# Optimization experiments

Measured on AMD Instinct MI355X. Metric: run time of the kernel, lower is better.

## Reference

```python
import jax, jax.numpy as jnp
import numpy as np

DIM = 3072
NUM_HEADS = 24
HEAD_DIM = DIM // NUM_HEADS        # 128
B = 1
F, H, W = 4, 24, 24
S = F * H * W                      # 2304
EPS = 1e-6
MAX_POS = 1024
C2 = HEAD_DIM // 2                 # 64 rotary channel-pairs per head
CF = C2 - 2 * (C2 // 3)            # 22 pairs for frame axis
CH = C2 // 3                       # 21 pairs each for H and W axes


def rmsnorm(x, g, eps=EPS):
    # fp32 RMSNorm over last dim with affine weight g [DIM]
    xf = x.astype(jnp.float32)
    ms = jnp.mean(xf * xf, axis=-1, keepdims=True)
    return (xf * jax.lax.rsqrt(ms + eps) * g).astype(x.dtype)


def apply_default_rope(x, grid_sizes, freqs):
    # x: [B, S, N, D]; freqs: [1024, C2] angle table; grid_sizes: [B,3] (F,H,W)
    b, s, n, d = x.shape
    gh = grid_sizes[0, 1]
    gw = grid_sizes[0, 2]
    pos = jnp.arange(s)
    fi = pos // (gh * gw)
    hi = (pos % (gh * gw)) // gw
    wi = pos % gw
    # per-position angles, split across (F, H, W) channel groups -> [S, C2]
    theta = jnp.concatenate([
        freqs[fi, :CF],
        freqs[hi, CF:CF + CH],
        freqs[wi, CF + CH:],
    ], axis=-1)
    cos = jnp.cos(theta)[None, :, None, :]
    sin = jnp.sin(theta)[None, :, None, :]
    xp = x.astype(jnp.float32).reshape(b, s, n, d // 2, 2)
    xr, xi = xp[..., 0], xp[..., 1]
    out = jnp.stack([xr * cos - xi * sin, xr * sin + xi * cos], axis=-1)
    return out.reshape(b, s, n, d).astype(x.dtype)


def setup_inputs() -> dict:
    key = jax.random.key(0)
    ks = jax.random.split(key, 10)
    def w(k):
        return jax.random.normal(k, (DIM, DIM), dtype=jnp.float32) * 0.02
    inv = 10000.0 ** (-jnp.arange(C2, dtype=jnp.float32) / C2)
    freqs = jnp.arange(MAX_POS, dtype=jnp.float32)[:, None] * inv[None, :]
    return {
        "x": jax.random.normal(ks[0], (B, S, DIM), dtype=jnp.float32),
        "seq_lens": jnp.full((B,), S, dtype=jnp.int32),
        "grid_sizes": jnp.tile(jnp.array([[F, H, W]], dtype=jnp.int32), (B, 1)),
        "freqs": freqs,
        "wq": w(ks[1]), "bq": jnp.zeros((DIM,), jnp.float32),
        "wk": w(ks[2]), "bk": jnp.zeros((DIM,), jnp.float32),
        "wv": w(ks[3]), "bv": jnp.zeros((DIM,), jnp.float32),
        "wo": w(ks[4]), "bo": jnp.zeros((DIM,), jnp.float32),
        "gq": jnp.ones((DIM,), jnp.float32),
        "gk": jnp.ones((DIM,), jnp.float32),
    }


def reference(x, seq_lens, grid_sizes, freqs, wq, bq, wk, bk, wv, bv, wo, bo, gq, gk):
    b, s = x.shape[:2]
    n, d = NUM_HEADS, HEAD_DIM
    # QKV projections (torch Linear: x @ W.T + b) + fp32 RMSNorm on q, k
    q = rmsnorm(x @ wq.T + bq, gq).reshape(b, s, n, d)
    k = rmsnorm(x @ wk.T + bk, gk).reshape(b, s, n, d)
    v = (x @ wv.T + bv).reshape(b, s, n, d)
    # 3-axis (F,H,W) RoPE on q, k
    q = apply_default_rope(q, grid_sizes, freqs)
    k = apply_default_rope(k, grid_sizes, freqs)
    # non-causal attention with k_lens masking
    scores = jnp.einsum('bqnd,bknd->bnqk', q, k) * (d ** -0.5)
    kmask = jnp.arange(s)[None, :] < seq_lens[:, None]          # [B, S]
    scores = jnp.where(kmask[:, None, None, :], scores, -1e9)
    probs = jax.nn.softmax(scores, axis=-1)
    out = jnp.einsum('bnqk,bknd->bqnd', probs, v).reshape(b, s, n * d)
    return out @ wo.T + bo
```

## Files before the change

### kernel.cpp

```cpp
#include <hip/hip_runtime.h>
#include <hip/hip_bf16.h>
#include <cstdint>

#define S_LEN 2304
#define NDIM  3072
#define NH    24
#define HD    128

typedef unsigned short u16;
typedef __bf16  bf16x8  __attribute__((ext_vector_type(8)));
typedef float   floatx4 __attribute__((ext_vector_type(4)));

__device__ __forceinline__ u16 f2bf(float x) {
  union { float f; unsigned int u; } a; a.f = x;
  unsigned int r = (a.u + 0x7FFFu + ((a.u >> 16) & 1u)) >> 16;
  return (u16)r;
}

__device__ __forceinline__ void async_load16(const void* g, void* l) {
  auto gp = (const __attribute__((address_space(1))) unsigned int*)(unsigned long long)(g);
  auto lp = (__attribute__((address_space(3))) unsigned int*)(unsigned int)(unsigned long long)(l);
  __builtin_amdgcn_global_load_lds(gp, lp, 16, 0, 0);
}

__global__ __launch_bounds__(256) void cvt_all(const float* __restrict__ x,
                                               const float* __restrict__ w0,
                                               const float* __restrict__ w1,
                                               const float* __restrict__ w2,
                                               const float* __restrict__ w3,
                                               u16* __restrict__ xo,
                                               u16* __restrict__ o0,
                                               u16* __restrict__ o1,
                                               u16* __restrict__ o2,
                                               u16* __restrict__ o3) {
  long b = blockIdx.x;
  const float* in; u16* out;
  if (b < 3456) { in = x; out = xo; }
  else {
    long wi = (b - 3456) / 4608;
    b = (b - 3456) % 4608;
    in  = (wi == 0) ? w0 : (wi == 1) ? w1 : (wi == 2) ? w2 : w3;
    out = (wi == 0) ? o0 : (wi == 1) ? o1 : (wi == 2) ? o2 : o3;
  }
  long i = (b * 256 + threadIdx.x) * 8;
  float4 a = *(const float4*)(in + i);
  float4 c = *(const float4*)(in + i + 4);
  union { u16 h[8]; uint4 u; } r;
  r.h[0] = f2bf(a.x); r.h[1] = f2bf(a.y); r.h[2] = f2bf(a.z); r.h[3] = f2bf(a.w);
  r.h[4] = f2bf(c.x); r.h[5] = f2bf(c.y); r.h[6] = f2bf(c.z); r.h[7] = f2bf(c.w);
  *(uint4*)(out + i) = r.u;
}

__device__ __forceinline__ void gemm_tile(const u16* __restrict__ A,
                                          const u16* __restrict__ B,
                                          const float* __restrict__ bias,
                                          float* __restrict__ C,
                                          int bm, int bn,
                                          u16* As, u16* Bs) {
  constexpr int N = NDIM, K = NDIM;
  const int t = threadIdx.x;
  const int l = t & 63, w = t >> 6;
  const int l15 = l & 15, quad = l >> 4;
  const int wm = (w >> 1) * 64, wn = (w & 1) * 64;

  floatx4 acc[4][4];
#pragma unroll
  for (int i = 0; i < 4; ++i)
#pragma unroll
    for (int j = 0; j < 4; ++j) acc[i][j] = {0.f, 0.f, 0.f, 0.f};

  for (int kt = 0; kt < K / 64; ++kt) {
    const int k0 = kt * 64;
#pragma unroll
    for (int i = 0; i < 4; ++i) {
      int p = i * 256 + t;
      int r = p >> 3;
      int c = (p & 7) ^ (r & 7);
      async_load16(A + (long)(bm + r) * K + k0 + c * 8, As + p * 8);
      async_load16(B + (long)(bn + r) * K + k0 + c * 8, Bs + p * 8);
    }
    __syncthreads();
#pragma unroll
    for (int kk = 0; kk < 2; ++kk) {
      bf16x8 af[4], bfr[4];
#pragma unroll
      for (int i = 0; i < 4; ++i) {
        int row = wm + i * 16 + l15;
        int cc = kk * 4 + quad;
        af[i] = *(const bf16x8*)(As + (row * 8 + (cc ^ (row & 7))) * 8);
      }
#pragma unroll
      for (int j = 0; j < 4; ++j) {
        int row = wn + j * 16 + l15;
        int cc = kk * 4 + quad;
        bfr[j] = *(const bf16x8*)(Bs + (row * 8 + (cc ^ (row & 7))) * 8);
      }
#pragma unroll
      for (int i = 0; i < 4; ++i)
#pragma unroll
        for (int j = 0; j < 4; ++j)
          acc[i][j] = __builtin_amdgcn_mfma_f32_16x16x32_bf16(af[i], bfr[j], acc[i][j], 0, 0, 0);
    }
    __syncthreads();
  }
#pragma unroll
  for (int i = 0; i < 4; ++i)
#pragma unroll
    for (int j = 0; j < 4; ++j) {
      int gm = bm + wm + i * 16 + quad * 4;
      int gn = bn + wn + j * 16 + l15;
      float bv = bias[gn];
#pragma unroll
      for (int r = 0; r < 4; ++r)
        C[(long)(gm + r) * N + gn] = acc[i][j][r] + bv;
    }
}

__global__ __launch_bounds__(256, 2) void gemm_qkv(const u16* __restrict__ A,
                                                   const u16* __restrict__ wq,
                                                   const u16* __restrict__ wk,
                                                   const u16* __restrict__ wv,
                                                   const float* __restrict__ bq,
                                                   const float* __restrict__ bk,
                                                   const float* __restrict__ bv,
                                                   float* __restrict__ qf,
                                                   float* __restrict__ kf,
                                                   float* __restrict__ vf) {
  __shared__ u16 As[128 * 64];
  __shared__ u16 Bs[128 * 64];
  const int sel = blockIdx.x / 24;
  const int bn = (blockIdx.x % 24) * 128;
  const int bm = blockIdx.y * 128;
  const u16*   B    = (sel == 0) ? wq : (sel == 1) ? wk : wv;
  const float* bias = (sel == 0) ? bq : (sel == 1) ? bk : bv;
  float*       C    = (sel == 0) ? qf : (sel == 1) ? kf : vf;
  gemm_tile(A, B, bias, C, bm, bn, As, Bs);
}

__global__ __launch_bounds__(256, 2) void gemm_bt(const u16* __restrict__ A,
                                                  const u16* __restrict__ B,
                                                  const float* __restrict__ bias,
                                                  float* __restrict__ C) {
  __shared__ u16 As[128 * 64];
  __shared__ u16 Bs[128 * 64];
  gemm_tile(A, B, bias, C, blockIdx.y * 128, blockIdx.x * 128, As, Bs);
}

__global__ __launch_bounds__(256) void rmsnorm_rope(const float* __restrict__ qxf,
                                                    const float* __restrict__ kxf,
                                                    const float* __restrict__ gqp,
                                                    const float* __restrict__ gkp,
                                                    const float* __restrict__ freqs,
                                                    const int* __restrict__ gsz,
                                                    u16* __restrict__ qop,
                                                    u16* __restrict__ kop) {
  const int tok = blockIdx.x;
  const int tid = threadIdx.x;
  const float* xf = blockIdx.y ? kxf : qxf;
  const float* g  = blockIdx.y ? gkp : gqp;
  u16* outp       = blockIdx.y ? kop : qop;
  const float* row = xf + (long)tok * NDIM;
  float4 v[3];
  float ss = 0.f;
#pragma unroll
  for (int p = 0; p < 3; ++p) {
    v[p] = ((const float4*)row)[p * 256 + tid];
    ss += v[p].x * v[p].x + v[p].y * v[p].y + v[p].z * v[p].z + v[p].w * v[p].w;
  }
#pragma unroll
  for (int m = 1; m < 64; m <<= 1) ss += __shfl_xor(ss, m);
  __shared__ float red[4];
  if ((tid & 63) == 0) red[tid >> 6] = ss;
  __syncthreads();
  ss = red[0] + red[1] + red[2] + red[3];
  const float scale = rsqrtf(ss * (1.0f / NDIM) + 1e-6f);

  const int gh = gsz[1], gw = gsz[2];
  const int hw = gh * gw;
  const int fi = tok / hw;
  const int hi = (tok % hw) / gw;
  const int wi = tok % gw;
#pragma unroll
  for (int p = 0; p < 3; ++p) {
    const int e0 = (p * 256 + tid) * 4;
    const float4 gg = ((const float4*)g)[p * 256 + tid];
    const int hh = e0 >> 7;
    const int d = e0 & 127;
    const int c0 = d >> 1;
    int pos0 = (c0 < 22) ? fi : ((c0 < 43) ? hi : wi);
    int pos1 = (c0 + 1 < 22) ? fi : ((c0 + 1 < 43) ? hi : wi);
    float th0 = freqs[pos0 * 64 + c0];
    float th1 = freqs[pos1 * 64 + c0 + 1];
    float s0, cc0, s1, cc1;
    __sincosf(th0, &s0, &cc0);
    __sincosf(th1, &s1, &cc1);
    float x0 = v[p].x * scale * gg.x;
    float x1 = v[p].y * scale * gg.y;
    float x2 = v[p].z * scale * gg.z;
    float x3 = v[p].w * scale * gg.w;
    union { u16 h[4]; uint2 u; } o;
    o.h[0] = f2bf(x0 * cc0 - x1 * s0);
    o.h[1] = f2bf(x0 * s0 + x1 * cc0);
    o.h[2] = f2bf(x2 * cc1 - x3 * s1);
    o.h[3] = f2bf(x2 * s1 + x3 * cc1);
    *(uint2*)(outp + ((long)hh * S_LEN + tok) * HD + d) = o.u;
  }
}

__global__ __launch_bounds__(256) void vtrans(const float* __restrict__ vf,
                                              u16* __restrict__ vt) {
  __shared__ float tile[64][65];
  const int c0 = blockIdx.x * 64;
  const int t0 = blockIdx.y * 64;
  const int tid = threadIdx.x;
#pragma unroll
  for (int it = 0; it < 16; ++it) {
    int idx = it * 256 + tid;
    int r = idx >> 6, c = idx & 63;
    tile[r][c] = vf[(long)(t0 + r) * NDIM + c0 + c];
  }
  __syncthreads();
#pragma unroll
  for (int it = 0; it < 16; ++it) {
    int idx = it * 256 + tid;
    int r = idx >> 6, c = idx & 63;
    vt[(long)(c0 + r) * S_LEN + t0 + c] = f2bf(tile[c][r]);
  }
}

__global__ __launch_bounds__(256, 2) void attn_kern(const u16* __restrict__ qb,
                                                    const u16* __restrict__ kb,
                                                    const u16* __restrict__ vt,
                                                    const int* __restrict__ seq_lens,
                                                    u16* __restrict__ ob) {
  __shared__ u16 Kb[2][64 * 128];
  __shared__ u16 Vb[2][128 * 64];
  __shared__ u16 Ps[128 * 64];
  const int b = blockIdx.x;
  const int xcd = b & 7;
  const int slot = b >> 3;
  const int h = xcd * 3 + slot / 18;
  const int qt = slot % 18;
  const int t = threadIdx.x;
  const int l = t & 63, w = t >> 6;
  const int l15 = l & 15, quad = l >> 4;
  const int seqlen = seq_lens[0];
  const float SC2 = 0.12753102543f;

  const u16* kbase = kb + (long)h * S_LEN * HD;
  const u16* vbase = vt + (long)h * HD * S_LEN;

  bf16x8 qfrag[2][4];
#pragma unroll
  for (int i = 0; i < 2; ++i) {
    const u16* qrow = qb + ((long)h * S_LEN + qt * 128 + w * 32 + i * 16 + l15) * HD + quad * 8;
#pragma unroll
    for (int kk = 0; kk < 4; ++kk) qfrag[i][kk] = *(const bf16x8*)(qrow + kk * 32);
  }

  bf16x8 ones;
#pragma unroll
  for (int i = 0; i < 8; ++i) ones[i] = (__bf16)1.0f;

  floatx4 oacc[2][8];
  floatx4 lacc[2];
#pragma unroll
  for (int i = 0; i < 2; ++i) {
#pragma unroll
    for (int j = 0; j < 8; ++j) oacc[i][j] = {0.f, 0.f, 0.f, 0.f};
    lacc[i] = {0.f, 0.f, 0.f, 0.f};
  }

  auto stage = [&](int kt, int buf) {
#pragma unroll
    for (int i = 0; i < 4; ++i) {
      int p = i * 256 + t;
      int rk = p >> 4;
      int ck = (p & 15) ^ (rk & 15);
      async_load16(kbase + ((long)(kt * 64 + rk)) * HD + ck * 8, &Kb[buf][p * 8]);
      int dv = p >> 3;
      int cv = (p & 7) ^ (dv & 7);
      async_load16(vbase + (long)dv * S_LEN + kt * 64 + cv * 8, &Vb[buf][p * 8]);
    }
  };

  stage(0, 0);

  for (int kt = 0; kt < S_LEN / 64; ++kt) {
    const int cur = kt & 1;
    __syncthreads();
    if (kt + 1 < S_LEN / 64) stage(kt + 1, cur ^ 1);

    floatx4 sacc[2][4];
#pragma unroll
    for (int i = 0; i < 2; ++i)
#pragma unroll
      for (int j = 0; j < 4; ++j) sacc[i][j] = {0.f, 0.f, 0.f, 0.f};
#pragma unroll
    for (int kk = 0; kk < 4; ++kk) {
#pragma unroll
      for (int j = 0; j < 4; ++j) {
        int row = j * 16 + l15;
        int cc = kk * 4 + quad;
        bf16x8 bk = *(const bf16x8*)(&Kb[cur][(row * 16 + (cc ^ (row & 15))) * 8]);
        sacc[0][j] = __builtin_amdgcn_mfma_f32_16x16x32_bf16(qfrag[0][kk], bk, sacc[0][j], 0, 0, 0);
        sacc[1][j] = __builtin_amdgcn_mfma_f32_16x16x32_bf16(qfrag[1][kk], bk, sacc[1][j], 0, 0, 0);
      }
    }

    const bool tail = (kt * 64 + 64 > seqlen);
#pragma unroll
    for (int i = 0; i < 2; ++i)
#pragma unroll
      for (int j = 0; j < 4; ++j)
#pragma unroll
        for (int r = 0; r < 4; ++r) {
          float sv = sacc[i][j][r] * SC2;
          if (tail) {
            int col = kt * 64 + j * 16 + l15;
            if (col >= seqlen) sv = -1e30f;
          }
          sacc[i][j][r] = exp2f(sv);
        }

#pragma unroll
    for (int i = 0; i < 2; ++i)
#pragma unroll
      for (int j = 0; j < 4; ++j)
#pragma unroll
        for (int r = 0; r < 4; ++r) {
          int rq = w * 32 + i * 16 + quad * 4 + r;
          int ct = j * 16 + l15;
          int cc = ct >> 3;
          Ps[(rq * 8 + (cc ^ (rq & 7))) * 8 + (ct & 7)] = f2bf(sacc[i][j][r]);
        }

#pragma unroll
    for (int kl = 0; kl < 2; ++kl) {
      bf16x8 ap[2];
#pragma unroll
      for (int i = 0; i < 2; ++i) {
        int row = w * 32 + i * 16 + l15;
        int cc = kl * 4 + quad;
        ap[i] = *(const bf16x8*)(&Ps[(row * 8 + (cc ^ (row & 7))) * 8]);
      }
      lacc[0] = __builtin_amdgcn_mfma_f32_16x16x32_bf16(ap[0], ones, lacc[0], 0, 0, 0);
      lacc[1] = __builtin_amdgcn_mfma_f32_16x16x32_bf16(ap[1], ones, lacc[1], 0, 0, 0);
#pragma unroll
      for (int j = 0; j < 8; ++j) {
        int d = j * 16 + l15;
        int ccv = kl * 4 + quad;
        bf16x8 bv = *(const bf16x8*)(&Vb[cur][(d * 8 + (ccv ^ (d & 7))) * 8]);
        oacc[0][j] = __builtin_amdgcn_mfma_f32_16x16x32_bf16(ap[0], bv, oacc[0][j], 0, 0, 0);
        oacc[1][j] = __builtin_amdgcn_mfma_f32_16x16x32_bf16(ap[1], bv, oacc[1][j], 0, 0, 0);
      }
    }
  }

#pragma unroll
  for (int i = 0; i < 2; ++i) {
    float inv[4];
#pragma unroll
    for (int r = 0; r < 4; ++r) inv[r] = 1.0f / lacc[i][r];
#pragma unroll
    for (int j = 0; j < 8; ++j) {
      int gt = qt * 128 + w * 32 + i * 16 + quad * 4;
      int gc = h * HD + j * 16 + l15;
#pragma unroll
      for (int r = 0; r < 4; ++r)
        ob[(long)(gt + r) * NDIM + gc] = f2bf(oacc[i][j][r] * inv[r]);
    }
  }
}

extern "C" void kernel_launch(void* const* d_in, const int* in_sizes, int n_in,
                              void* d_out, int out_size, void* d_ws, size_t ws_size,
                              hipStream_t stream) {
  const float* x        = (const float*)d_in[0];
  const int*   seq_lens = (const int*)  d_in[1];
  const int*   gsz      = (const int*)  d_in[2];
  const float* freqs    = (const float*)d_in[3];
  const float* wq       = (const float*)d_in[4];
  const float* bq       = (const float*)d_in[5];
  const float* wk       = (const float*)d_in[6];
  const float* bk       = (const float*)d_in[7];
  const float* wv       = (const float*)d_in[8];
  const float* bv       = (const float*)d_in[9];
  const float* wo       = (const float*)d_in[10];
  const float* bo       = (const float*)d_in[11];
  const float* gq       = (const float*)d_in[12];
  const float* gk       = (const float*)d_in[13];
  float* out = (float*)d_out;

  char* ws = (char*)d_ws;
  const size_t SD2 = (size_t)S_LEN * NDIM * 2;
  const size_t W2  = (size_t)NDIM * NDIM * 2;
  const size_t SD4 = (size_t)S_LEN * NDIM * 4;
  size_t off = 0;
  u16* xb    = (u16*)(ws + off); off += SD2;
  u16* wqb   = (u16*)(ws + off); off += W2;
  u16* wkb   = (u16*)(ws + off); off += W2;
  u16* wvb   = (u16*)(ws + off); off += W2;
  u16* wob   = (u16*)(ws + off); off += W2;
  float* qf  = (float*)(ws + off); off += SD4;
  float* kf  = (float*)(ws + off); off += SD4;
  float* vf  = (float*)(ws + off); off += SD4;
  u16* qbuf  = (u16*)(ws + off); off += SD2;
  u16* kbuf  = (u16*)(ws + off); off += SD2;
  u16* vtb   = (u16*)(ws + off); off += SD2;
  u16* attnb = (u16*)(ws + off); off += SD2;

  cvt_all<<<3456 + 4 * 4608, 256, 0, stream>>>(x, wq, wk, wv, wo,
                                               xb, wqb, wkb, wvb, wob);

  gemm_qkv<<<dim3(72, 18), 256, 0, stream>>>(xb, wqb, wkb, wvb,
                                             bq, bk, bv, qf, kf, vf);

  rmsnorm_rope<<<dim3(S_LEN, 2), 256, 0, stream>>>(qf, kf, gq, gk, freqs, gsz,
                                                   qbuf, kbuf);
  vtrans<<<dim3(NDIM / 64, S_LEN / 64), 256, 0, stream>>>(vf, vtb);

  attn_kern<<<432, 256, 0, stream>>>(qbuf, kbuf, vtb, seq_lens, attnb);

  gemm_bt<<<dim3(NDIM / 128, S_LEN / 128), 256, 0, stream>>>(attnb, wob, bo, out);
}
```

Baseline: 575.1 us.

## Double-buffer GEMMs with 256x128 tiles, XCD swizzle, and bf16 V output

Replaces the single-buffered 128x128 GEMM tile with a 512-thread, 256x128 tile that double-buffers LDS loads. The next K-slice is prefetched while MFMAs run, using explicit vmcnt waits and setprio. Block indices are remapped so neighbouring tiles land on the same XCD, which should improve L2 reuse. The V projection now writes bf16 directly, which halves the traffic into the transpose kernel. In exchange, LDS use per block doubles, which may lower occupancy, and the grid has fewer, larger blocks.

```diff
diff --git a/kernel.cpp b/kernel.cpp
--- a/kernel.cpp
+++ b/kernel.cpp
@@ -51,72 +51,79 @@
   *(uint4*)(out + i) = r.u;
 }
 
-__device__ __forceinline__ void gemm_tile(const u16* __restrict__ A,
-                                          const u16* __restrict__ B,
-                                          const float* __restrict__ bias,
-                                          float* __restrict__ C,
-                                          int bm, int bn,
-                                          u16* As, u16* Bs) {
-  constexpr int N = NDIM, K = NDIM;
+__device__ __forceinline__ void gemm_core_256x128(const u16* __restrict__ A,
+                                                  const u16* __restrict__ Bw,
+                                                  int bm, int bn,
+                                                  u16 (*As)[256 * 64],
+                                                  u16 (*Bs)[128 * 64],
+                                                  floatx4 acc[4][4]) {
+  constexpr int NT = NDIM / 64;
   const int t = threadIdx.x;
-  const int l = t & 63, w = t >> 6;
+  const int l = t & 63;
+  const int w = t >> 6;
   const int l15 = l & 15, quad = l >> 4;
   const int wm = (w >> 1) * 64, wn = (w & 1) * 64;
 
-  floatx4 acc[4][4];
+  const int rb = t >> 3;
+  const int ch = (t & 7) ^ (rb & 7);
+  const u16* aSrc = A  + (long)(bm + rb) * NDIM + ch * 8;
+  const u16* bSrc = Bw + (long)(bn + rb) * NDIM + ch * 8;
+
+  const int s0 = quad ^ (l15 & 7);
+
 #pragma unroll
   for (int i = 0; i < 4; ++i)
 #pragma unroll
     for (int j = 0; j < 4; ++j) acc[i][j] = {0.f, 0.f, 0.f, 0.f};
 
-  for (int kt = 0; kt < K / 64; ++kt) {
+  auto stage = [&](int kt, int buf) {
     const int k0 = kt * 64;
 #pragma unroll
-    for (int i = 0; i < 4; ++i) {
-      int p = i * 256 + t;
-      int r = p >> 3;
-      int c = (p & 7) ^ (r & 7);
-      async_load16(A + (long)(bm + r) * K + k0 + c * 8, As + p * 8);
-      async_load16(B + (long)(bn + r) * K + k0 + c * 8, Bs + p * 8);
-    }
-    __syncthreads();
+    for (int i = 0; i < 4; ++i)
+      async_load16(aSrc + (long)i * 64 * NDIM + k0, &As[buf][(i * 512 + t) * 8]);
+#pragma unroll
+    for (int i = 0; i < 2; ++i)
+      async_load16(bSrc + (long)i * 64 * NDIM + k0, &Bs[buf][(i * 512 + t) * 8]);
+  };
+
+  stage(0, 0);
+
+  for (int kt = 0; kt < NT; ++kt) {
+    const int cur = kt & 1;
+    __builtin_amdgcn_sched_barrier(0);
+    __builtin_amdgcn_s_barrier();
+    __builtin_amdgcn_sched_barrier(0);
+    if (kt + 1 < NT) {
+      stage(kt + 1, cur ^ 1);
+      asm volatile("s_waitcnt vmcnt(6)" ::: "memory");
+    } else {
+      asm volatile("s_waitcnt vmcnt(0)" ::: "memory");
+    }
+    __builtin_amdgcn_sched_barrier(0);
+    __builtin_amdgcn_s_barrier();
+    __builtin_amdgcn_sched_barrier(0);
 #pragma unroll
     for (int kk = 0; kk < 2; ++kk) {
+      const int sw = s0 ^ (kk << 2);
       bf16x8 af[4], bfr[4];
 #pragma unroll
-      for (int i = 0; i < 4; ++i) {
-        int row = wm + i * 16 + l15;
-        int cc = kk * 4 + quad;
-        af[i] = *(const bf16x8*)(As + (row * 8 + (cc ^ (row & 7))) * 8);
-      }
-#pragma unroll
-      for (int j = 0; j < 4; ++j) {
-        int row = wn + j * 16 + l15;
-        int cc = kk * 4 + quad;
-        bfr[j] = *(const bf16x8*)(Bs + (row * 8 + (cc ^ (row & 7))) * 8);
-      }
+      for (int i = 0; i < 4; ++i)
+        af[i] = *(const bf16x8*)(&As[cur][(wm + i * 16 + l15) * 64 + sw * 8]);
+#pragma unroll
+      for (int j = 0; j < 4; ++j)
+        bfr[j] = *(const bf16x8*)(&Bs[cur][(wn + j * 16 + l15) * 64 + sw * 8]);
+      __builtin_amdgcn_s_setprio(1);
 #pragma unroll
       for (int i = 0; i < 4; ++i)
 #pragma unroll
         for (int j = 0; j < 4; ++j)
           acc[i][j] = __builtin_amdgcn_mfma_f32_16x16x32_bf16(af[i], bfr[j], acc[i][j], 0, 0, 0);
-    }
-    __syncthreads();
-  }
-#pragma unroll
-  for (int i = 0; i < 4; ++i)
-#pragma unroll
-    for (int j = 0; j < 4; ++j) {
-      int gm = bm + wm + i * 16 + quad * 4;
-      int gn = bn + wn + j * 16 + l15;
-      float bv = bias[gn];
-#pragma unroll
-      for (int r = 0; r < 4; ++r)
-        C[(long)(gm + r) * N + gn] = acc[i][j][r] + bv;
-    }
-}
-
-__global__ __launch_bounds__(256, 2) void gemm_qkv(const u16* __restrict__ A,
+      __builtin_amdgcn_s_setprio(0);
+    }
+  }
+}
+
+__global__ __launch_bounds__(512, 2) void gemm_qkv(const u16* __restrict__ A,
                                                    const u16* __restrict__ wq,
                                                    const u16* __restrict__ wk,
                                                    const u16* __restrict__ wv,
@@ -125,25 +132,89 @@
                                                    const float* __restrict__ bv,
                                                    float* __restrict__ qf,
                                                    float* __restrict__ kf,
-                                                   float* __restrict__ vf) {
-  __shared__ u16 As[128 * 64];
-  __shared__ u16 Bs[128 * 64];
-  const int sel = blockIdx.x / 24;
-  const int bn = (blockIdx.x % 24) * 128;
-  const int bm = blockIdx.y * 128;
-  const u16*   B    = (sel == 0) ? wq : (sel == 1) ? wk : wv;
+                                                   u16* __restrict__ vbf) {
+  __shared__ u16 As[2][256 * 64];
+  __shared__ u16 Bs[2][128 * 64];
+  const int bid = blockIdx.x;
+  const int swz = (bid & 7) * 81 + (bid >> 3);
+  const int tm = swz / 72;
+  const int tn = swz % 72;
+  const int sel = tn / 24;
+  const int bn = (tn % 24) * 128;
+  const int bm = tm * 256;
+  const u16* Bw = (sel == 0) ? wq : (sel == 1) ? wk : wv;
+
+  floatx4 acc[4][4];
+  gemm_core_256x128(A, Bw, bm, bn, As, Bs, acc);
+
+  const int t = threadIdx.x;
+  const int l = t & 63, w = t >> 6;
+  const int l15 = l & 15, quad = l >> 4;
+  const int wm = (w >> 1) * 64, wn = (w & 1) * 64;
   const float* bias = (sel == 0) ? bq : (sel == 1) ? bk : bv;
-  float*       C    = (sel == 0) ? qf : (sel == 1) ? kf : vf;
-  gemm_tile(A, B, bias, C, bm, bn, As, Bs);
-}
-
-__global__ __launch_bounds__(256, 2) void gemm_bt(const u16* __restrict__ A,
-                                                  const u16* __restrict__ B,
+
+  if (sel < 2) {
+    float* C = sel ? kf : qf;
+#pragma unroll
+    for (int i = 0; i < 4; ++i) {
+      const int gm = bm + wm + i * 16 + quad * 4;
+#pragma unroll
+      for (int j = 0; j < 4; ++j) {
+        const int gn = bn + wn + j * 16 + l15;
+        const float bb = bias[gn];
+#pragma unroll
+        for (int r = 0; r < 4; ++r)
+          C[(long)(gm + r) * NDIM + gn] = acc[i][j][r] + bb;
+      }
+    }
+  } else {
+#pragma unroll
+    for (int i = 0; i < 4; ++i) {
+      const int gm = bm + wm + i * 16 + quad * 4;
+#pragma unroll
+      for (int j = 0; j < 4; ++j) {
+        const int gn = bn + wn + j * 16 + l15;
+        const float bb = bias[gn];
+#pragma unroll
+        for (int r = 0; r < 4; ++r)
+          vbf[(long)(gm + r) * NDIM + gn] = f2bf(acc[i][j][r] + bb);
+      }
+    }
+  }
+}
+
+__global__ __launch_bounds__(512, 2) void gemm_bt(const u16* __restrict__ A,
+                                                  const u16* __restrict__ Bw,
                                                   const float* __restrict__ bias,
                                                   float* __restrict__ C) {
-  __shared__ u16 As[128 * 64];
-  __shared__ u16 Bs[128 * 64];
-  gemm_tile(A, B, bias, C, blockIdx.y * 128, blockIdx.x * 128, As, Bs);
+  __shared__ u16 As[2][256 * 64];
+  __shared__ u16 Bs[2][128 * 64];
+  const int bid = blockIdx.x;
+  const int swz = (bid & 7) * 27 + (bid >> 3);
+  const int tm = swz / 24;
+  const int tn = swz % 24;
+  const int bm = tm * 256;
+  const int bn = tn * 128;
+
+  floatx4 acc[4][4];
+  gemm_core_256x128(A, Bw, bm, bn, As, Bs, acc);
+
+  const int t = threadIdx.x;
+  const int l = t & 63, w = t >> 6;
+  const int l15 = l & 15, quad = l >> 4;
+  const int wm = (w >> 1) * 64, wn = (w & 1) * 64;
+#pragma unroll
+  for (int i = 0; i < 4; ++i) {
+    const int gm = bm + wm + i * 16 + quad * 4;
+#pragma unroll
+    for (int j = 0; j < 4; ++j) {
+      const int gn = bn + wn + j * 16 + l15;
+      const float bb = bias[gn];
+#pragma unroll
+      for (int r = 0; r < 4; ++r)
+        C[(long)(gm + r) * NDIM + gn] = acc[i][j][r] + bb;
+    }
+  }
 }
 
 __global__ __launch_bounds__(256) void rmsnorm_rope(const float* __restrict__ qxf,
@@ -207,9 +278,9 @@
   }
 }
 
-__global__ __launch_bounds__(256) void vtrans(const float* __restrict__ vf,
+__global__ __launch_bounds__(256) void vtrans(const u16* __restrict__ vb,
                                               u16* __restrict__ vt) {
-  __shared__ float tile[64][65];
+  __shared__ u16 tile[64][66];
   const int c0 = blockIdx.x * 64;
   const int t0 = blockIdx.y * 64;
   const int tid = threadIdx.x;
@@ -217,14 +288,14 @@
   for (int it = 0; it < 16; ++it) {
     int idx = it * 256 + tid;
     int r = idx >> 6, c = idx & 63;
-    tile[r][c] = vf[(long)(t0 + r) * NDIM + c0 + c];
+    tile[r][c] = vb[(long)(t0 + r) * NDIM + c0 + c];
   }
   __syncthreads();
 #pragma unroll
   for (int it = 0; it < 16; ++it) {
     int idx = it * 256 + tid;
     int r = idx >> 6, c = idx & 63;
-    vt[(long)(c0 + r) * S_LEN + t0 + c] = f2bf(tile[c][r]);
+    vt[(long)(c0 + r) * S_LEN + t0 + c] = tile[c][r];
   }
 }
 
@@ -404,7 +475,7 @@
   u16* wob   = (u16*)(ws + off); off += W2;
   float* qf  = (float*)(ws + off); off += SD4;
   float* kf  = (float*)(ws + off); off += SD4;
-  float* vf  = (float*)(ws + off); off += SD4;
+  u16* vbf   = (u16*)(ws + off); off += SD4;
   u16* qbuf  = (u16*)(ws + off); off += SD2;
   u16* kbuf  = (u16*)(ws + off); off += SD2;
   u16* vtb   = (u16*)(ws + off); off += SD2;
@@ -413,14 +484,14 @@
   cvt_all<<<3456 + 4 * 4608, 256, 0, stream>>>(x, wq, wk, wv, wo,
                                                xb, wqb, wkb, wvb, wob);
 
-  gemm_qkv<<<dim3(72, 18), 256, 0, stream>>>(xb, wqb, wkb, wvb,
-                                             bq, bk, bv, qf, kf, vf);
+  gemm_qkv<<<648, 512, 0, stream>>>(xb, wqb, wkb, wvb,
+                                    bq, bk, bv, qf, kf, vbf);
 
   rmsnorm_rope<<<dim3(S_LEN, 2), 256, 0, stream>>>(qf, kf, gq, gk, freqs, gsz,
                                                    qbuf, kbuf);
-  vtrans<<<dim3(NDIM / 64, S_LEN / 64), 256, 0, stream>>>(vf, vtb);
+  vtrans<<<dim3(NDIM / 64, S_LEN / 64), 256, 0, stream>>>(vbf, vtb);
 
   attn_kern<<<432, 256, 0, stream>>>(qbuf, kbuf, vtb, seq_lens, attnb);
 
-  gemm_bt<<<dim3(NDIM / 128, S_LEN / 128), 256, 0, stream>>>(attnb, wob, bo, out);
-}
+  gemm_bt<<<216, 512, 0, stream>>>(attnb, wob, bo, out);
+}
```

Result: no change. 571.8 us (-0.6%).
